# Performance work log

Measured on AMD Instinct MI355X. Metric: run time of the kernel, lower is better.

Reference implementation:

```python
import jax, jax.numpy as jnp
import numpy as np

N, E = 50000, 800000
NF, EF, S = 128, 64, 128

def _lin(key, fan_in, fan_out):
    k1, k2 = jax.random.split(key)
    lim = 1.0 / np.sqrt(fan_in)
    W = jax.random.uniform(k1, (fan_in, fan_out), jnp.float32, -lim, lim)
    b = jax.random.uniform(k2, (fan_out,), jnp.float32, -lim, lim)
    return W, b

def setup_inputs() -> dict:
    key = jax.random.key(0)
    ks = jax.random.split(key, 12)
    x = jax.random.normal(ks[0], (N, NF), jnp.float32)
    edge_index = jax.random.randint(ks[1], (2, E), 0, N, jnp.int64)
    edge_attr = jax.random.normal(ks[2], (E, EF), jnp.float32)
    Wn, bn = _lin(ks[3], NF, S)
    We, be = _lin(ks[4], EF, S)
    Wzc, bzc = _lin(ks[5], S, S)   # GCNConv weight/bias (z gate)
    Wzl, bzl = _lin(ks[6], 2 * S, S)
    Wrc, brc = _lin(ks[7], S, S)
    Wrl, brl = _lin(ks[8], 2 * S, S)
    Whc, bhc = _lin(ks[9], S, S)
    Whl, bhl = _lin(ks[10], 2 * S, S)
    Wout, bout = _lin(ks[11], 3 * S, 1)
    return dict(x=x, edge_index=edge_index, edge_attr=edge_attr,
                Wn=Wn, bn=bn, We=We, be=be,
                Wzc=Wzc, bzc=bzc, Wzl=Wzl, bzl=bzl,
                Wrc=Wrc, brc=brc, Wrl=Wrl, brl=brl,
                Whc=Whc, bhc=bhc, Whl=Whl, bhl=bhl,
                Wout=Wout, bout=bout)

def reference(x, edge_index, edge_attr, Wn, bn, We, be,
              Wzc, bzc, Wzl, bzl, Wrc, brc, Wrl, brl,
              Whc, bhc, Whl, bhl, Wout, bout):
    n = x.shape[0]
    src, dst = edge_index[0], edge_index[1]
    xe = jax.nn.relu(x @ Wn + bn)                      # [N,S]
    ea = jax.nn.relu(edge_attr @ We + be)              # [E,S]
    # GCNConv normalization with self-loops (shared across the 3 gates)
    loop = jnp.arange(n)
    s2 = jnp.concatenate([src, loop])
    d2 = jnp.concatenate([dst, loop])
    deg = jax.ops.segment_sum(jnp.ones(s2.shape[0], xe.dtype), d2, n)
    dinv = jax.lax.rsqrt(deg)                          # deg >= 1 (self loops)
    norm = (dinv[s2] * dinv[d2])[:, None]              # [E+N,1]
    def gcn(W, b):
        xw = xe @ W
        return jax.ops.segment_sum(xw[s2] * norm, d2, n) + b
    H = jnp.zeros_like(xe)
    Z = jax.nn.sigmoid(jnp.concatenate([gcn(Wzc, bzc), H], 1) @ Wzl + bzl)
    R = jax.nn.sigmoid(jnp.concatenate([gcn(Wrc, brc), H], 1) @ Wrl + brl)
    Ht = jnp.tanh(jnp.concatenate([gcn(Whc, bhc), H * R], 1) @ Whl + bhl)
    H = Z * H + (1.0 - Z) * Ht                          # [N,S]
    edge_h = jnp.concatenate([H[src], H[dst], ea], axis=1)  # [E,3S]
    return edge_h @ Wout + bout                         # [E,1]
```

## Files before the change

### kernel.cpp

```cpp
#include <hip/hip_runtime.h>
#include <hip/hip_bf16.h>
#include <math.h>

#define NN 50000
#define EE 800000

typedef __bf16 bf16x8 __attribute__((ext_vector_type(8)));
typedef float f32x4 __attribute__((ext_vector_type(4)));
typedef unsigned int u32x4 __attribute__((ext_vector_type(4)));

#define G1B 3253
__global__ __launch_bounds__(256) void k_fused0(const int* __restrict__ ei, int* __restrict__ deg,
                            const float* __restrict__ Wzc, const float* __restrict__ bzc,
                            const float* __restrict__ Wzl, const float* __restrict__ bzl,
                            const float* __restrict__ Whc, const float* __restrict__ bhc,
                            const float* __restrict__ Whl, const float* __restrict__ bhl,
                            float* __restrict__ Wcat, float* __restrict__ cb,
                            const float* __restrict__ x, const float* __restrict__ Wn,
                            const float* __restrict__ bn, __hip_bfloat16* __restrict__ xs) {
    if (blockIdx.x < 128) {
        int i = blockIdx.x;
        int k = threadIdx.x;
        if (k < 128) {
            float sz = 0.f, sh = 0.f;
            for (int j = 0; j < 128; j++) {
                sz += Wzc[i * 128 + j] * Wzl[j * 128 + k];
                sh += Whc[i * 128 + j] * Whl[j * 128 + k];
            }
            Wcat[i * 256 + 2 * k]     = sz;
            Wcat[i * 256 + 2 * k + 1] = sh;
            if (i == 0) {
                float bz = bzl[k], bh = bhl[k];
                for (int j = 0; j < 128; j++) {
                    bz += bzc[j] * Wzl[j * 128 + k];
                    bh += bhc[j] * Whl[j * 128 + k];
                }
                cb[2 * k]     = bz;
                cb[2 * k + 1] = bh;
            }
        }
    } else if (blockIdx.x < G1B) {
        int e = (blockIdx.x - 128) * 256 + threadIdx.x;
        if (e < EE) atomicAdd(&deg[ei[EE + e]], 1);
    } else {
        const int lane = threadIdx.x & 63;
        const int ln = lane & 15;
        const int q  = lane >> 4;
        const int wid = ((blockIdx.x - G1B) * 256 + threadIdx.x) >> 6;
        const int nw  = (gridDim.x - G1B) * 4;
        const int ch  = wid & 1;
        const int step = nw >> 1;

        bf16x8 bfrag[4][4];
#pragma unroll
        for (int t = 0; t < 4; t++)
#pragma unroll
            for (int kc = 0; kc < 4; kc++)
#pragma unroll
                for (int j = 0; j < 8; j++)
                    bfrag[t][kc][j] = (__bf16)Wn[(kc * 32 + q * 8 + j) * 128 + ch * 64 + t * 16 + ln];
        float biasR[4];
#pragma unroll
        for (int t = 0; t < 4; t++) biasR[t] = bn[ch * 64 + t * 16 + ln];

        for (int rt = wid >> 1; rt < 3125; rt += step) {
            const int e0 = rt * 16;
            const float* arow = x + (size_t)(e0 + ln) * 128;
            bf16x8 af[4];
#pragma unroll
            for (int kc = 0; kc < 4; kc++) {
                float4 v0 = *(const float4*)(arow + kc * 32 + q * 8);
                float4 v1 = *(const float4*)(arow + kc * 32 + q * 8 + 4);
                af[kc][0] = (__bf16)v0.x; af[kc][1] = (__bf16)v0.y;
                af[kc][2] = (__bf16)v0.z; af[kc][3] = (__bf16)v0.w;
                af[kc][4] = (__bf16)v1.x; af[kc][5] = (__bf16)v1.y;
                af[kc][6] = (__bf16)v1.z; af[kc][7] = (__bf16)v1.w;
            }
            f32x4 acc[4];
#pragma unroll
            for (int t = 0; t < 4; t++) acc[t] = (f32x4){0.f, 0.f, 0.f, 0.f};
#pragma unroll
            for (int t = 0; t < 4; t++)
#pragma unroll
                for (int kc = 0; kc < 4; kc++)
                    acc[t] = __builtin_amdgcn_mfma_f32_16x16x32_bf16(af[kc], bfrag[t][kc], acc[t], 0, 0, 0);
#pragma unroll
            for (int t = 0; t < 4; t++)
#pragma unroll
                for (int r = 0; r < 4; r++) {
                    float v = fmaxf(acc[t][r] + biasR[t], 0.f);
                    xs[(size_t)(e0 + q * 4 + r) * 128 + ch * 64 + t * 16 + ln] = __float2bfloat16(v);
                }
        }
    }
}

__global__ void k_scan_a(const int* __restrict__ deg, int* __restrict__ partial) {
    __shared__ int s[256];
    int i = blockIdx.x * 256 + threadIdx.x;
    s[threadIdx.x] = (i < NN) ? deg[i] : 0;
    __syncthreads();
    for (int off = 128; off > 0; off >>= 1) {
        if (threadIdx.x < off) s[threadIdx.x] += s[threadIdx.x + off];
        __syncthreads();
    }
    if (threadIdx.x == 0) partial[blockIdx.x] = s[0];
}

__global__ void k_scan_c(const int* __restrict__ deg, const int* __restrict__ partial,
                         int* __restrict__ rowptr, int* __restrict__ cursor,
                         float* __restrict__ dinvArr) {
    __shared__ int s[256];
    __shared__ int ps[256];
    int i = blockIdx.x * 256 + threadIdx.x;
    int v = (i < NN) ? deg[i] : 0;
    s[threadIdx.x] = v;
    ps[threadIdx.x] = (threadIdx.x < blockIdx.x) ? partial[threadIdx.x] : 0;
    __syncthreads();
    for (int off = 128; off > 0; off >>= 1) {
        if (threadIdx.x < off) ps[threadIdx.x] += ps[threadIdx.x + off];
        __syncthreads();
    }
    for (int off = 1; off < 256; off <<= 1) {
        int t = (threadIdx.x >= off) ? s[threadIdx.x - off] : 0;
        __syncthreads();
        s[threadIdx.x] += t;
        __syncthreads();
    }
    int excl = s[threadIdx.x] - v + ps[0];
    if (i < NN) {
        rowptr[i] = excl; cursor[i] = excl;
        dinvArr[i] = rsqrtf((float)(v + 1));
    }
    if (i == 0) rowptr[NN] = EE;
}

__global__ void k_fill(const int* __restrict__ ei, int* __restrict__ cursor,
                       int* __restrict__ col) {
    int e = blockIdx.x * 256 + threadIdx.x;
    if (e < EE) {
        int d = ei[EE + e];
        int p = atomicAdd(&cursor[d], 1);
        col[p] = ei[e];
    }
}

__global__ __launch_bounds__(256) void k_gather(const unsigned int* __restrict__ xsu,
                                                const int* __restrict__ rowptr,
                                                const int* __restrict__ col,
                                                const float* __restrict__ dinvArr,
                                                unsigned int* __restrict__ aggu) {
    int gt = blockIdx.x * 256 + threadIdx.x;
    int node = gt >> 6;
    int lane = threadIdx.x & 63;
    if (node >= NN) return;
    const int g = lane >> 4;
    const int k = lane & 15;
    int beg = rowptr[node], end = rowptr[node + 1];
    const float dn = dinvArr[node];

    float acc[8];
#pragma unroll
    for (int i = 0; i < 8; i++) acc[i] = 0.f;

    {
        u32x4 sv = *(const u32x4*)(xsu + (size_t)node * 64 + k * 4);
        if (g == 0) {
#pragma unroll
            for (int d = 0; d < 4; d++) {
                acc[2 * d]     += dn * __uint_as_float(sv[d] << 16);
                acc[2 * d + 1] += dn * __uint_as_float(sv[d] & 0xFFFF0000u);
            }
        }
    }

    int p = beg;
    while (p < end) {
        int rem = end - p;
        int chunk = rem < 64 ? rem : 64;
        int cv = (lane < chunk) ? col[p + lane] : 0;
        for (int j = 0; j < chunk; j += 4) {
            int s = __shfl(cv, j + g);
            float dv = dinvArr[s];
            u32x4 v = *(const u32x4*)(xsu + (size_t)s * 64 + k * 4);
            if (j + g >= chunk) v = (u32x4){0u, 0u, 0u, 0u};
#pragma unroll
            for (int d = 0; d < 4; d++) {
                acc[2 * d]     += dv * __uint_as_float(v[d] << 16);
                acc[2 * d + 1] += dv * __uint_as_float(v[d] & 0xFFFF0000u);
            }
        }
        p += 64;
    }

#pragma unroll
    for (int off = 16; off < 64; off <<= 1)
#pragma unroll
        for (int i = 0; i < 8; i++) acc[i] += __shfl_xor(acc[i], off);

    unsigned int o0, o1, o2, o3;
    {
        __hip_bfloat16 lo, hi;
        lo = __float2bfloat16(acc[0] * dn); hi = __float2bfloat16(acc[1] * dn);
        o0 = (unsigned int)*(unsigned short*)&lo | ((unsigned int)*(unsigned short*)&hi << 16);
        lo = __float2bfloat16(acc[2] * dn); hi = __float2bfloat16(acc[3] * dn);
        o1 = (unsigned int)*(unsigned short*)&lo | ((unsigned int)*(unsigned short*)&hi << 16);
        lo = __float2bfloat16(acc[4] * dn); hi = __float2bfloat16(acc[5] * dn);
        o2 = (unsigned int)*(unsigned short*)&lo | ((unsigned int)*(unsigned short*)&hi << 16);
        lo = __float2bfloat16(acc[6] * dn); hi = __float2bfloat16(acc[7] * dn);
        o3 = (unsigned int)*(unsigned short*)&lo | ((unsigned int)*(unsigned short*)&hi << 16);
    }
    int src = lane >> 2;
    unsigned int t0 = __shfl((int)o0, src);
    unsigned int t1 = __shfl((int)o1, src);
    unsigned int t2 = __shfl((int)o2, src);
    unsigned int t3 = __shfl((int)o3, src);
    int c2 = lane & 3;
    unsigned int res = (c2 == 0) ? t0 : (c2 == 1) ? t1 : (c2 == 2) ? t2 : t3;
    aggu[(size_t)node * 64 + lane] = res;
}

__global__ __launch_bounds__(256) void k_gate_red(const unsigned int* __restrict__ aggu,
                                                  const float* __restrict__ Wcat,
                                                  const float* __restrict__ cb,
                                                  const float* __restrict__ Wout,
                                                  float* __restrict__ aArr,
                                                  float* __restrict__ bArr) {
    __shared__ float red[4][32];
    const int lane = threadIdx.x & 63;
    const int ln = lane & 15;
    const int q  = lane >> 4;
    const int w  = threadIdx.x >> 6;

    bf16x8 bfrag[4][4];
#pragma unroll
    for (int t = 0; t < 4; t++)
#pragma unroll
        for (int kc = 0; kc < 4; kc++)
#pragma unroll
            for (int j = 0; j < 8; j++)
                bfrag[t][kc][j] = (__bf16)Wcat[(kc * 32 + q * 8 + j) * 256 + w * 64 + t * 16 + ln];

    float cbR[4], wAR[4], wBR[4];
#pragma unroll
    for (int t = 0; t < 4; t++) {
        int c = w * 64 + t * 16 + ln;
        cbR[t] = cb[c];
        int k = c >> 1;
        wAR[t] = Wout[k];
        wBR[t] = Wout[128 + k];
    }
    const bool odd = (ln & 1);

    for (int rt = blockIdx.x; rt < 3125; rt += gridDim.x) {
        const int e0 = rt * 16;
        const u32x4* arow = (const u32x4*)aggu + (size_t)(e0 + ln) * 16;
        bf16x8 af[4];
#pragma unroll
        for (int kc = 0; kc < 4; kc++) {
            u32x4 uv = arow[kc * 4 + q];
            af[kc] = __builtin_bit_cast(bf16x8, uv);
        }
        f32x4 acc[4];
#pragma unroll
        for (int t = 0; t < 4; t++) acc[t] = (f32x4){0.f, 0.f, 0.f, 0.f};
#pragma unroll
        for (int t = 0; t < 4; t++)
#pragma unroll
            for (int kc = 0; kc < 4; kc++)
                acc[t] = __builtin_amdgcn_mfma_f32_16x16x32_bf16(af[kc], bfrag[t][kc], acc[t], 0, 0, 0);

        float pa[4] = {0.f, 0.f, 0.f, 0.f};
        float pb[4] = {0.f, 0.f, 0.f, 0.f};
#pragma unroll
        for (int t = 0; t < 4; t++)
#pragma unroll
            for (int r = 0; r < 4; r++) {
                float val = acc[t][r] + cbR[t];
                float s = odd ? tanhf(val) : (1.f / (1.f + expf(-val)));
                float partner = __shfl_xor(s, 1);
                if (!odd) {
                    float h = (1.f - s) * partner;
                    pa[r] += h * wAR[t];
                    pb[r] += h * wBR[t];
                }
            }
#pragma unroll
        for (int off = 1; off < 16; off <<= 1) {
#pragma unroll
            for (int r = 0; r < 4; r++) {
                pa[r] += __shfl_xor(pa[r], off);
                pb[r] += __shfl_xor(pb[r], off);
            }
        }
        if (ln < 4) {
            float v = (ln == 0) ? pa[0] : (ln == 1) ? pa[1] : (ln == 2) ? pa[2] : pa[3];
            red[w][q * 4 + ln] = v;
        } else if (ln < 8) {
            int r = ln - 4;
            float v = (r == 0) ? pb[0] : (r == 1) ? pb[1] : (r == 2) ? pb[2] : pb[3];
            red[w][16 + q * 4 + r] = v;
        }
        __syncthreads();
        if (threadIdx.x < 32) {
            int row = threadIdx.x & 15;
            int ab = threadIdx.x >> 4;
            float s = red[0][ab * 16 + row] + red[1][ab * 16 + row]
                    + red[2][ab * 16 + row] + red[3][ab * 16 + row];
            if (ab) bArr[e0 + row] = s; else aArr[e0 + row] = s;
        }
        __syncthreads();
    }
}

__global__ __launch_bounds__(256) void k_edge_mfma(const float* __restrict__ EA,
                                                   const int* __restrict__ ei,
                                                   const float* __restrict__ We,
                                                   const float* __restrict__ be,
                                                   const float* __restrict__ Wout,
                                                   const float* __restrict__ boutp,
                                                   const float* __restrict__ aArr,
                                                   const float* __restrict__ bArr,
                                                   float* __restrict__ out) {
    const int lane = threadIdx.x & 63;
    const int ln = lane & 15;
    const int q  = lane >> 4;
    const int wid = (blockIdx.x * 256 + threadIdx.x) >> 6;
    const int nw  = gridDim.x * 4;

    bf16x8 bfrag[2][8];
#pragma unroll
    for (int h = 0; h < 2; h++)
#pragma unroll
        for (int t = 0; t < 8; t++)
#pragma unroll
            for (int j = 0; j < 8; j++)
                bfrag[h][t][j] = (__bf16)We[(h * 32 + q * 8 + j) * 128 + t * 16 + ln];

    float beR[8], w3R[8];
#pragma unroll
    for (int t = 0; t < 8; t++) {
        beR[t] = be[t * 16 + ln];
        w3R[t] = Wout[256 + t * 16 + ln];
    }
    const float b0 = boutp[0];

    for (int tile = wid; tile < EE / 16; tile += nw) {
        const int e0 = tile * 16;
        const float* arow = EA + (size_t)(e0 + ln) * 64;
        float4 v0 = *(const float4*)(arow + q * 8);
        float4 v1 = *(const float4*)(arow + q * 8 + 4);
        float4 v2 = *(const float4*)(arow + 32 + q * 8);
        float4 v3 = *(const float4*)(arow + 32 + q * 8 + 4);
        bf16x8 af0, af1;
        af0[0] = (__bf16)v0.x; af0[1] = (__bf16)v0.y; af0[2] = (__bf16)v0.z; af0[3] = (__bf16)v0.w;
        af0[4] = (__bf16)v1.x; af0[5] = (__bf16)v1.y; af0[6] = (__bf16)v1.z; af0[7] = (__bf16)v1.w;
        af1[0] = (__bf16)v2.x; af1[1] = (__bf16)v2.y; af1[2] = (__bf16)v2.z; af1[3] = (__bf16)v2.w;
        af1[4] = (__bf16)v3.x; af1[5] = (__bf16)v3.y; af1[6] = (__bf16)v3.z; af1[7] = (__bf16)v3.w;

        f32x4 acc[8];
#pragma unroll
        for (int t = 0; t < 8; t++) acc[t] = (f32x4){0.f, 0.f, 0.f, 0.f};
#pragma unroll
        for (int t = 0; t < 8; t++)
            acc[t] = __builtin_amdgcn_mfma_f32_16x16x32_bf16(af0, bfrag[0][t], acc[t], 0, 0, 0);
#pragma unroll
        for (int t = 0; t < 8; t++)
            acc[t] = __builtin_amdgcn_mfma_f32_16x16x32_bf16(af1, bfrag[1][t], acc[t], 0, 0, 0);

        float part[4] = {0.f, 0.f, 0.f, 0.f};
#pragma unroll
        for (int t = 0; t < 8; t++)
#pragma unroll
            for (int r = 0; r < 4; r++) {
                float y = acc[t][r] + beR[t];
                y = fmaxf(y, 0.f);
                part[r] += y * w3R[t];
            }
#pragma unroll
        for (int off = 1; off < 16; off <<= 1) {
#pragma unroll
            for (int r = 0; r < 4; r++) part[r] += __shfl_xor(part[r], off);
        }
        if (ln < 4) {
            float c = (ln == 0) ? part[0] : (ln == 1) ? part[1] : (ln == 2) ? part[2] : part[3];
            int e = e0 + q * 4 + ln;
            out[e] = c + aArr[ei[e]] + bArr[ei[EE + e]] + b0;
        }
    }
}

extern "C" void kernel_launch(void* const* d_in, const int* in_sizes, int n_in,
                              void* d_out, int out_size, void* d_ws, size_t ws_size,
                              hipStream_t stream) {
    const float* x    = (const float*)d_in[0];
    const int*   ei   = (const int*)d_in[1];
    const float* ea   = (const float*)d_in[2];
    const float* Wn   = (const float*)d_in[3];
    const float* bn   = (const float*)d_in[4];
    const float* We   = (const float*)d_in[5];
    const float* be   = (const float*)d_in[6];
    const float* Wzc  = (const float*)d_in[7];
    const float* bzc  = (const float*)d_in[8];
    const float* Wzl  = (const float*)d_in[9];
    const float* bzl  = (const float*)d_in[10];
    const float* Whc  = (const float*)d_in[15];
    const float* bhc  = (const float*)d_in[16];
    const float* Whl  = (const float*)d_in[17];
    const float* bhl  = (const float*)d_in[18];
    const float* Wout = (const float*)d_in[19];
    const float* bout = (const float*)d_in[20];
    float* out = (float*)d_out;

    char* w = (char*)d_ws;
    auto carve = [&](size_t bytes) {
        void* p = (void*)w;
        w += (bytes + 255) / 256 * 256;
        return p;
    };
    int*   deg     = (int*)carve((size_t)NN * 4);
    float* aArr    = (float*)carve((size_t)NN * 4);
    float* bArr    = (float*)carve((size_t)NN * 4);
    float* dinvArr = (float*)carve((size_t)NN * 4);
    __hip_bfloat16* xs = (__hip_bfloat16*)carve((size_t)NN * 128 * 2);
    unsigned int* aggu = (unsigned int*)carve((size_t)NN * 64 * 4);
    float* Wcat    = (float*)carve(128 * 256 * 4);
    float* cb      = (float*)carve(256 * 4);
    int*   rowptr  = (int*)carve((size_t)(NN + 1) * 4);
    int*   cursor  = (int*)carve((size_t)NN * 4);
    int*   col     = (int*)carve((size_t)EE * 4);
    int*   partial = (int*)carve(256 * 4);

    hipMemsetAsync(deg, 0, (size_t)NN * 4, stream);

    k_fused0<<<G1B + 768, 256, 0, stream>>>(ei, deg, Wzc, bzc, Wzl, bzl,
                                            Whc, bhc, Whl, bhl, Wcat, cb,
                                            x, Wn, bn, xs);

    const int NB = (NN + 255) / 256;
    k_scan_a<<<NB, 256, 0, stream>>>(deg, partial);
    k_scan_c<<<NB, 256, 0, stream>>>(deg, partial, rowptr, cursor, dinvArr);
    k_fill<<<3125, 256, 0, stream>>>(ei, cursor, col);

    k_gather<<<(NN * 64 + 255) / 256, 256, 0, stream>>>((const unsigned int*)xs, rowptr, col, dinvArr, aggu);

    k_gate_red<<<512, 256, 0, stream>>>(aggu, Wcat, cb, Wout, aArr, bArr);

    k_edge_mfma<<<2048, 256, 0, stream>>>(ea, ei, We, be, Wout, bout, aArr, bArr, out);
}
```

Before: 514.5 us.

## Move edge-attr MLP into first fused kernel, add node terms in light pass

Moves the edge-attribute MFMA projection and its Wout dot product out of the last kernel and into the first fused kernel. It now runs in parallel with degree counting, the node projection and the weight folding, using interleaved odd/even block roles. The final kernel shrinks to a simple gather-add of the per-node a/b terms into out. This overlaps the heavy edge GEMM with independent early work and takes it off the critical tail of the dependency chain. The cost is an extra read-modify-write pass over out, and a larger first kernel whose register use is set by the heaviest branch.

```diff
diff --git a/kernel.cpp b/kernel.cpp
--- a/kernel.cpp
+++ b/kernel.cpp
@@ -9,7 +9,7 @@
 typedef float f32x4 __attribute__((ext_vector_type(4)));
 typedef unsigned int u32x4 __attribute__((ext_vector_type(4)));
 
-#define G1B 3253
+#define GRID0 6506
 __global__ __launch_bounds__(256) void k_fused0(const int* __restrict__ ei, int* __restrict__ deg,
                             const float* __restrict__ Wzc, const float* __restrict__ bzc,
                             const float* __restrict__ Wzl, const float* __restrict__ bzl,
@@ -17,80 +17,155 @@
                             const float* __restrict__ Whl, const float* __restrict__ bhl,
                             float* __restrict__ Wcat, float* __restrict__ cb,
                             const float* __restrict__ x, const float* __restrict__ Wn,
-                            const float* __restrict__ bn, __hip_bfloat16* __restrict__ xs) {
-    if (blockIdx.x < 128) {
-        int i = blockIdx.x;
-        int k = threadIdx.x;
-        if (k < 128) {
-            float sz = 0.f, sh = 0.f;
-            for (int j = 0; j < 128; j++) {
-                sz += Wzc[i * 128 + j] * Wzl[j * 128 + k];
-                sh += Whc[i * 128 + j] * Whl[j * 128 + k];
-            }
-            Wcat[i * 256 + 2 * k]     = sz;
-            Wcat[i * 256 + 2 * k + 1] = sh;
-            if (i == 0) {
-                float bz = bzl[k], bh = bhl[k];
+                            const float* __restrict__ bn, __hip_bfloat16* __restrict__ xs,
+                            const float* __restrict__ EA, const float* __restrict__ We,
+                            const float* __restrict__ be, const float* __restrict__ Wout,
+                            const float* __restrict__ boutp, float* __restrict__ out) {
+    const unsigned B = blockIdx.x;
+    const unsigned v = B >> 1;
+    if (B & 1u) {
+        if (v < 2048) {
+            const int lane = threadIdx.x & 63;
+            const int ln = lane & 15;
+            const int q  = lane >> 4;
+            const int wid = v * 4 + (threadIdx.x >> 6);
+            const int nw  = 8192;
+
+            bf16x8 bfrag[2][8];
+#pragma unroll
+            for (int h = 0; h < 2; h++)
+#pragma unroll
+                for (int t = 0; t < 8; t++)
+#pragma unroll
+                    for (int j = 0; j < 8; j++)
+                        bfrag[h][t][j] = (__bf16)We[(h * 32 + q * 8 + j) * 128 + t * 16 + ln];
+
+            float beR[8], w3R[8];
+#pragma unroll
+            for (int t = 0; t < 8; t++) {
+                beR[t] = be[t * 16 + ln];
+                w3R[t] = Wout[256 + t * 16 + ln];
+            }
+            const float b0 = boutp[0];
+
+            for (int tile = wid; tile < EE / 16; tile += nw) {
+                const int e0 = tile * 16;
+                const float* arow = EA + (size_t)(e0 + ln) * 64;
+                float4 v0 = *(const float4*)(arow + q * 8);
+                float4 v1 = *(const float4*)(arow + q * 8 + 4);
+                float4 v2 = *(const float4*)(arow + 32 + q * 8);
+                float4 v3 = *(const float4*)(arow + 32 + q * 8 + 4);
+                bf16x8 af0, af1;
+                af0[0] = (__bf16)v0.x; af0[1] = (__bf16)v0.y; af0[2] = (__bf16)v0.z; af0[3] = (__bf16)v0.w;
+                af0[4] = (__bf16)v1.x; af0[5] = (__bf16)v1.y; af0[6] = (__bf16)v1.z; af0[7] = (__bf16)v1.w;
+                af1[0] = (__bf16)v2.x; af1[1] = (__bf16)v2.y; af1[2] = (__bf16)v2.z; af1[3] = (__bf16)v2.w;
+                af1[4] = (__bf16)v3.x; af1[5] = (__bf16)v3.y; af1[6] = (__bf16)v3.z; af1[7] = (__bf16)v3.w;
+
+                f32x4 acc[8];
+#pragma unroll
+                for (int t = 0; t < 8; t++) acc[t] = (f32x4){0.f, 0.f, 0.f, 0.f};
+#pragma unroll
+                for (int t = 0; t < 8; t++)
+                    acc[t] = __builtin_amdgcn_mfma_f32_16x16x32_bf16(af0, bfrag[0][t], acc[t], 0, 0, 0);
+#pragma unroll
+                for (int t = 0; t < 8; t++)
+                    acc[t] = __builtin_amdgcn_mfma_f32_16x16x32_bf16(af1, bfrag[1][t], acc[t], 0, 0, 0);
+
+                float part[4] = {0.f, 0.f, 0.f, 0.f};
+#pragma unroll
+                for (int t = 0; t < 8; t++)
+#pragma unroll
+                    for (int r = 0; r < 4; r++) {
+                        float y = acc[t][r] + beR[t];
+                        y = fmaxf(y, 0.f);
+                        part[r] += y * w3R[t];
+                    }
+#pragma unroll
+                for (int off = 1; off < 16; off <<= 1) {
+#pragma unroll
+                    for (int r = 0; r < 4; r++) part[r] += __shfl_xor(part[r], off);
+                }
+                if (ln < 4) {
+                    float c = (ln == 0) ? part[0] : (ln == 1) ? part[1] : (ln == 2) ? part[2] : part[3];
+                    out[e0 + q * 4 + ln] = c + b0;
+                }
+            }
+        } else if (v < 2816) {
+            const int lane = threadIdx.x & 63;
+            const int ln = lane & 15;
+            const int q  = lane >> 4;
+            const int wid = (int)(v - 2048) * 4 + (threadIdx.x >> 6);
+            const int nw  = 3072;
+            const int ch  = wid & 1;
+            const int step = nw >> 1;
+
+            bf16x8 bfrag[4][4];
+#pragma unroll
+            for (int t = 0; t < 4; t++)
+#pragma unroll
+                for (int kc = 0; kc < 4; kc++)
+#pragma unroll
+                    for (int j = 0; j < 8; j++)
+                        bfrag[t][kc][j] = (__bf16)Wn[(kc * 32 + q * 8 + j) * 128 + ch * 64 + t * 16 + ln];
+            float biasR[4];
+#pragma unroll
+            for (int t = 0; t < 4; t++) biasR[t] = bn[ch * 64 + t * 16 + ln];
+
+            for (int rt = wid >> 1; rt < 3125; rt += step) {
+                const int e0 = rt * 16;
+                const float* arow = x + (size_t)(e0 + ln) * 128;
+                bf16x8 af[4];
+#pragma unroll
+                for (int kc = 0; kc < 4; kc++) {
+                    float4 v0 = *(const float4*)(arow + kc * 32 + q * 8);
+                    float4 v1 = *(const float4*)(arow + kc * 32 + q * 8 + 4);
+                    af[kc][0] = (__bf16)v0.x; af[kc][1] = (__bf16)v0.y;
+                    af[kc][2] = (__bf16)v0.z; af[kc][3] = (__bf16)v0.w;
+                    af[kc][4] = (__bf16)v1.x; af[kc][5] = (__bf16)v1.y;
+                    af[kc][6] = (__bf16)v1.z; af[kc][7] = (__bf16)v1.w;
+                }
+                f32x4 acc[4];
+#pragma unroll
+                for (int t = 0; t < 4; t++) acc[t] = (f32x4){0.f, 0.f, 0.f, 0.f};
+#pragma unroll
+                for (int t = 0; t < 4; t++)
+#pragma unroll
+                    for (int kc = 0; kc < 4; kc++)
+                        acc[t] = __builtin_amdgcn_mfma_f32_16x16x32_bf16(af[kc], bfrag[t][kc], acc[t], 0, 0, 0);
+#pragma unroll
+                for (int t = 0; t < 4; t++)
+#pragma unroll
+                    for (int r = 0; r < 4; r++) {
+                        float vv = fmaxf(acc[t][r] + biasR[t], 0.f);
+                        xs[(size_t)(e0 + q * 4 + r) * 128 + ch * 64 + t * 16 + ln] = __float2bfloat16(vv);
+                    }
+            }
+        }
+    } else {
+        if (v < 3125) {
+            int e = (int)v * 256 + threadIdx.x;
+            if (e < EE) atomicAdd(&deg[ei[EE + e]], 1);
+        } else {
+            int i = (int)v - 3125;
+            int k = threadIdx.x;
+            if (k < 128) {
+                float sz = 0.f, sh = 0.f;
                 for (int j = 0; j < 128; j++) {
-                    bz += bzc[j] * Wzl[j * 128 + k];
-                    bh += bhc[j] * Whl[j * 128 + k];
-                }
-                cb[2 * k]     = bz;
-                cb[2 * k + 1] = bh;
-            }
-        }
-    } else if (blockIdx.x < G1B) {
-        int e = (blockIdx.x - 128) * 256 + threadIdx.x;
-        if (e < EE) atomicAdd(&deg[ei[EE + e]], 1);
-    } else {
-        const int lane = threadIdx.x & 63;
-        const int ln = lane & 15;
-        const int q  = lane >> 4;
-        const int wid = ((blockIdx.x - G1B) * 256 + threadIdx.x) >> 6;
-        const int nw  = (gridDim.x - G1B) * 4;
-        const int ch  = wid & 1;
-        const int step = nw >> 1;
-
-        bf16x8 bfrag[4][4];
-#pragma unroll
-        for (int t = 0; t < 4; t++)
-#pragma unroll
-            for (int kc = 0; kc < 4; kc++)
-#pragma unroll
-                for (int j = 0; j < 8; j++)
-                    bfrag[t][kc][j] = (__bf16)Wn[(kc * 32 + q * 8 + j) * 128 + ch * 64 + t * 16 + ln];
-        float biasR[4];
-#pragma unroll
-        for (int t = 0; t < 4; t++) biasR[t] = bn[ch * 64 + t * 16 + ln];
-
-        for (int rt = wid >> 1; rt < 3125; rt += step) {
-            const int e0 = rt * 16;
-            const float* arow = x + (size_t)(e0 + ln) * 128;
-            bf16x8 af[4];
-#pragma unroll
-            for (int kc = 0; kc < 4; kc++) {
-                float4 v0 = *(const float4*)(arow + kc * 32 + q * 8);
-                float4 v1 = *(const float4*)(arow + kc * 32 + q * 8 + 4);
-                af[kc][0] = (__bf16)v0.x; af[kc][1] = (__bf16)v0.y;
-                af[kc][2] = (__bf16)v0.z; af[kc][3] = (__bf16)v0.w;
-                af[kc][4] = (__bf16)v1.x; af[kc][5] = (__bf16)v1.y;
-                af[kc][6] = (__bf16)v1.z; af[kc][7] = (__bf16)v1.w;
-            }
-            f32x4 acc[4];
-#pragma unroll
-            for (int t = 0; t < 4; t++) acc[t] = (f32x4){0.f, 0.f, 0.f, 0.f};
-#pragma unroll
-            for (int t = 0; t < 4; t++)
-#pragma unroll
-                for (int kc = 0; kc < 4; kc++)
-                    acc[t] = __builtin_amdgcn_mfma_f32_16x16x32_bf16(af[kc], bfrag[t][kc], acc[t], 0, 0, 0);
-#pragma unroll
-            for (int t = 0; t < 4; t++)
-#pragma unroll
-                for (int r = 0; r < 4; r++) {
-                    float v = fmaxf(acc[t][r] + biasR[t], 0.f);
-                    xs[(size_t)(e0 + q * 4 + r) * 128 + ch * 64 + t * 16 + ln] = __float2bfloat16(v);
-                }
+                    sz += Wzc[i * 128 + j] * Wzl[j * 128 + k];
+                    sh += Whc[i * 128 + j] * Whl[j * 128 + k];
+                }
+                Wcat[i * 256 + 2 * k]     = sz;
+                Wcat[i * 256 + 2 * k + 1] = sh;
+                if (i == 0) {
+                    float bz = bzl[k], bh = bhl[k];
+                    for (int j = 0; j < 128; j++) {
+                        bz += bzc[j] * Wzl[j * 128 + k];
+                        bh += bhc[j] * Whl[j * 128 + k];
+                    }
+                    cb[2 * k]     = bz;
+                    cb[2 * k + 1] = bh;
+                }
+            }
         }
     }
 }
@@ -313,81 +388,12 @@
     }
 }
 
-__global__ __launch_bounds__(256) void k_edge_mfma(const float* __restrict__ EA,
-                                                   const int* __restrict__ ei,
-                                                   const float* __restrict__ We,
-                                                   const float* __restrict__ be,
-                                                   const float* __restrict__ Wout,
-                                                   const float* __restrict__ boutp,
-                                                   const float* __restrict__ aArr,
-                                                   const float* __restrict__ bArr,
-                                                   float* __restrict__ out) {
-    const int lane = threadIdx.x & 63;
-    const int ln = lane & 15;
-    const int q  = lane >> 4;
-    const int wid = (blockIdx.x * 256 + threadIdx.x) >> 6;
-    const int nw  = gridDim.x * 4;
-
-    bf16x8 bfrag[2][8];
-#pragma unroll
-    for (int h = 0; h < 2; h++)
-#pragma unroll
-        for (int t = 0; t < 8; t++)
-#pragma unroll
-            for (int j = 0; j < 8; j++)
-                bfrag[h][t][j] = (__bf16)We[(h * 32 + q * 8 + j) * 128 + t * 16 + ln];
-
-    float beR[8], w3R[8];
-#pragma unroll
-    for (int t = 0; t < 8; t++) {
-        beR[t] = be[t * 16 + ln];
-        w3R[t] = Wout[256 + t * 16 + ln];
-    }
-    const float b0 = boutp[0];
-
-    for (int tile = wid; tile < EE / 16; tile += nw) {
-        const int e0 = tile * 16;
-        const float* arow = EA + (size_t)(e0 + ln) * 64;
-        float4 v0 = *(const float4*)(arow + q * 8);
-        float4 v1 = *(const float4*)(arow + q * 8 + 4);
-        float4 v2 = *(const float4*)(arow + 32 + q * 8);
-        float4 v3 = *(const float4*)(arow + 32 + q * 8 + 4);
-        bf16x8 af0, af1;
-        af0[0] = (__bf16)v0.x; af0[1] = (__bf16)v0.y; af0[2] = (__bf16)v0.z; af0[3] = (__bf16)v0.w;
-        af0[4] = (__bf16)v1.x; af0[5] = (__bf16)v1.y; af0[6] = (__bf16)v1.z; af0[7] = (__bf16)v1.w;
-        af1[0] = (__bf16)v2.x; af1[1] = (__bf16)v2.y; af1[2] = (__bf16)v2.z; af1[3] = (__bf16)v2.w;
-        af1[4] = (__bf16)v3.x; af1[5] = (__bf16)v3.y; af1[6] = (__bf16)v3.z; af1[7] = (__bf16)v3.w;
-
-        f32x4 acc[8];
-#pragma unroll
-        for (int t = 0; t < 8; t++) acc[t] = (f32x4){0.f, 0.f, 0.f, 0.f};
-#pragma unroll
-        for (int t = 0; t < 8; t++)
-            acc[t] = __builtin_amdgcn_mfma_f32_16x16x32_bf16(af0, bfrag[0][t], acc[t], 0, 0, 0);
-#pragma unroll
-        for (int t = 0; t < 8; t++)
-            acc[t] = __builtin_amdgcn_mfma_f32_16x16x32_bf16(af1, bfrag[1][t], acc[t], 0, 0, 0);
-
-        float part[4] = {0.f, 0.f, 0.f, 0.f};
-#pragma unroll
-        for (int t = 0; t < 8; t++)
-#pragma unroll
-            for (int r = 0; r < 4; r++) {
-                float y = acc[t][r] + beR[t];
-                y = fmaxf(y, 0.f);
-                part[r] += y * w3R[t];
-            }
-#pragma unroll
-        for (int off = 1; off < 16; off <<= 1) {
-#pragma unroll
-            for (int r = 0; r < 4; r++) part[r] += __shfl_xor(part[r], off);
-        }
-        if (ln < 4) {
-            float c = (ln == 0) ? part[0] : (ln == 1) ? part[1] : (ln == 2) ? part[2] : part[3];
-            int e = e0 + q * 4 + ln;
-            out[e] = c + aArr[ei[e]] + bArr[ei[EE + e]] + b0;
-        }
-    }
+__global__ void k_edge_add(const int* __restrict__ ei,
+                           const float* __restrict__ aArr,
+                           const float* __restrict__ bArr,
+                           float* __restrict__ out) {
+    int e = blockIdx.x * 256 + threadIdx.x;
+    if (e < EE) out[e] += aArr[ei[e]] + bArr[ei[EE + e]];
 }
 
 extern "C" void kernel_launch(void* const* d_in, const int* in_sizes, int n_in,
@@ -433,9 +439,10 @@
 
     hipMemsetAsync(deg, 0, (size_t)NN * 4, stream);
 
-    k_fused0<<<G1B + 768, 256, 0, stream>>>(ei, deg, Wzc, bzc, Wzl, bzl,
-                                            Whc, bhc, Whl, bhl, Wcat, cb,
-                                            x, Wn, bn, xs);
+    k_fused0<<<GRID0, 256, 0, stream>>>(ei, deg, Wzc, bzc, Wzl, bzl,
+                                        Whc, bhc, Whl, bhl, Wcat, cb,
+                                        x, Wn, bn, xs,
+                                        ea, We, be, Wout, bout, out);
 
     const int NB = (NN + 255) / 256;
     k_scan_a<<<NB, 256, 0, stream>>>(deg, partial);
@@ -446,5 +453,5 @@
 
     k_gate_red<<<512, 256, 0, stream>>>(aggu, Wcat, cb, Wout, aArr, bArr);
 
-    k_edge_mfma<<<2048, 256, 0, stream>>>(ea, ei, We, be, Wout, bout, aArr, bArr, out);
-}
+    k_edge_add<<<3125, 256, 0, stream>>>(ei, aArr, bArr, out);
+}
```

After: 543.9 us. +5.7%, slower.
